# Optimization experiments

Hardware: AMD Instinct MI355X
Metric: run time of the kernel (lower is better)

Reference implementation:

```python
import jax, jax.numpy as jnp
import numpy as np

EMB = 384
H = 6
D = 64
B = 256
T = 256


def setup_inputs() -> dict:
    key = jax.random.key(0)
    ks = jax.random.split(key, 6)
    s = 1.0 / np.sqrt(EMB)
    return {
        "x": jax.random.normal(ks[0], (B, T, EMB), dtype=jnp.float32),
        "wq": jax.random.normal(ks[1], (H, EMB, D), dtype=jnp.float32) * s,
        "wk": jax.random.normal(ks[2], (H, EMB, D), dtype=jnp.float32) * s,
        "wv": jax.random.normal(ks[3], (H, EMB, D), dtype=jnp.float32) * s,
        "w_proj": jax.random.normal(ks[4], (H * D, EMB), dtype=jnp.float32) * s,
        "b_proj": jax.random.normal(ks[5], (EMB,), dtype=jnp.float32) * 0.01,
    }


def reference(x, wq, wk, wv, w_proj, b_proj):
    # x: [B, T, E]; per-head projections stacked over H (dropout in eval mode)
    q = jnp.einsum("bte,hed->bhtd", x, wq)
    k = jnp.einsum("bte,hed->bhtd", x, wk)
    v = jnp.einsum("bte,hed->bhtd", x, wv)
    scale = q.shape[-1] ** -0.5
    scores = jnp.einsum("bhqd,bhkd->bhqk", q, k) * scale  # [B,H,T,T]
    tq = q.shape[2]
    causal = jnp.tril(jnp.ones((tq, tq), dtype=bool))
    scores = jnp.where(causal, scores, -jnp.inf)
    att = jax.nn.softmax(scores, axis=-1)
    out = jnp.einsum("bhqk,bhkd->bhqd", att, v)  # [B,H,T,D]
    out = out.transpose(0, 2, 1, 3).reshape(x.shape[0], tq, -1)  # concat heads
    return out @ w_proj + b_proj
```

## Files before the change

### kernel.cpp

```cpp
#include <hip/hip_runtime.h>
#include <hip/hip_bf16.h>


#define Bn 256
#define Tn 256
#define En 384
#define Hn 6
#define Dn 64

typedef __bf16 bf16x8 __attribute__((ext_vector_type(8)));
typedef float f32x4 __attribute__((ext_vector_type(4)));
typedef unsigned short u16x8 __attribute__((ext_vector_type(8)));

static __device__ __forceinline__ unsigned short f2bf(float f) {
    unsigned int u = __builtin_bit_cast(unsigned int, f);
    u += 0x7fffu + ((u >> 16) & 1u);
    return (unsigned short)(u >> 16);
}

static __device__ __forceinline__ f32x4 mfma16(bf16x8 a, bf16x8 b, f32x4 c) {
    return __builtin_amdgcn_mfma_f32_16x16x32_bf16(a, b, c, 0, 0, 0);
}

static __device__ __forceinline__ void glds16(const unsigned short* g, unsigned short* l) {
    __builtin_amdgcn_global_load_lds(
        (const __attribute__((address_space(1))) unsigned int*)g,
        (__attribute__((address_space(3))) unsigned int*)l, 16, 0, 0);
}

__global__ __launch_bounds__(256) void prep_kernel(
    const float* __restrict__ wq, const float* __restrict__ wk,
    const float* __restrict__ wv, const float* __restrict__ wp,
    unsigned short* __restrict__ wt, unsigned short* __restrict__ wpt) {
    const int NW = 3 * Hn * Dn * En;
    const int NP = En * En;
    int idx = blockIdx.x * 256 + threadIdx.x;
    if (idx < NW) {
        int e = idx % En;
        int d = (idx / En) % Dn;
        int h = (idx / (En * Dn)) % Hn;
        int t = idx / (En * Dn * Hn);
        const float* src = (t == 0) ? wq : (t == 1) ? wk : wv;
        wt[idx] = f2bf(src[(h * En + e) * Dn + d]);
    } else if (idx < NW + NP) {
        int j = idx - NW;
        int k = j % En;
        int n = j / En;
        wpt[j] = f2bf(wp[k * En + n]);
    }
}

__global__ __launch_bounds__(256) void xcast_kernel(
    const float* __restrict__ x, unsigned short* __restrict__ xb) {
    size_t i = ((size_t)blockIdx.x * 256 + threadIdx.x) * 8;
    float4 f0 = *(const float4*)(x + i);
    float4 f1 = *(const float4*)(x + i + 4);
    u16x8 p;
    p[0] = f2bf(f0.x); p[1] = f2bf(f0.y); p[2] = f2bf(f0.z); p[3] = f2bf(f0.w);
    p[4] = f2bf(f1.x); p[5] = f2bf(f1.y); p[6] = f2bf(f1.z); p[7] = f2bf(f1.w);
    *(u16x8*)(xb + i) = p;
}

__global__ __launch_bounds__(256) void qkv_gemm(
    const unsigned short* __restrict__ xb, const unsigned short* __restrict__ wt,
    unsigned short* __restrict__ Qo, unsigned short* __restrict__ Ko,
    unsigned short* __restrict__ Vt) {
    __shared__ unsigned short As[2][128][64];
    __shared__ unsigned short Bs[2][192][64];

    const int h = blockIdx.x;
    const int m0 = blockIdx.y * 128;

    const int tid = threadIdx.x;
    const int wave = tid >> 6, lane = tid & 63;
    const int quad = lane >> 4, l16 = lane & 15;
    const int mw = (wave >> 1) * 64, nw = (wave & 1) * 96;

    f32x4 acc[4][6];
#pragma unroll
    for (int i = 0; i < 4; ++i)
#pragma unroll
        for (int j = 0; j < 6; ++j) acc[i][j] = (f32x4){0.f, 0.f, 0.f, 0.f};

    const int lr = lane >> 3;
    const int js = (lane & 7) ^ lr;

    const unsigned short* ga[4];
#pragma unroll
    for (int i = 0; i < 4; ++i)
        ga[i] = xb + (size_t)(m0 + wave * 32 + i * 8 + lr) * En + js * 8;
    const unsigned short* gb[6];
#pragma unroll
    for (int i = 0; i < 6; ++i) {
        int n = wave * 48 + i * 8 + lr;
        gb[i] = wt + (size_t)(((n >> 6) * Hn + h) * Dn + (n & 63)) * En + js * 8;
    }

#define QKV_STAGE(buf, koff)                                              \
    do {                                                                  \
        _Pragma("unroll") for (int i = 0; i < 4; ++i)                     \
            glds16(ga[i] + (koff), &As[buf][wave * 32 + i * 8][0]);       \
        _Pragma("unroll") for (int i = 0; i < 6; ++i)                     \
            glds16(gb[i] + (koff), &Bs[buf][wave * 48 + i * 8][0]);       \
    } while (0)

    QKV_STAGE(0, 0);
    __syncthreads();

    int cur = 0;
    for (int kb = 0; kb < 6; ++kb) {
        if (kb < 5) QKV_STAGE(cur ^ 1, (kb + 1) * 64);

#pragma unroll
        for (int ks = 0; ks < 2; ++ks) {
            bf16x8 a[4], b[6];
            const int ps = ((ks * 4 + quad) ^ (l16 & 7)) * 8;
#pragma unroll
            for (int mi = 0; mi < 4; ++mi)
                a[mi] = *(const bf16x8*)&As[cur][mw + mi * 16 + l16][ps];
#pragma unroll
            for (int ni = 0; ni < 6; ++ni)
                b[ni] = *(const bf16x8*)&Bs[cur][nw + ni * 16 + l16][ps];
#pragma unroll
            for (int mi = 0; mi < 4; ++mi)
#pragma unroll
                for (int ni = 0; ni < 6; ++ni) acc[mi][ni] = mfma16(a[mi], b[ni], acc[mi][ni]);
        }
        if (kb < 5) {
            __syncthreads();
            cur ^= 1;
        }
    }
#undef QKV_STAGE

    const int b = m0 >> 8, tbase = m0 & 255;
    unsigned short* qkbase[2] = {
        Qo + (size_t)((b * Hn + h) * Tn) * Dn,
        Ko + (size_t)((b * Hn + h) * Tn) * Dn };
    unsigned short* vdst = Vt + (size_t)((b * Hn + h) * Dn) * Tn;
#pragma unroll
    for (int ni = 0; ni < 6; ++ni) {
        const int ng = nw + ni * 16;
        const int tensor = ng >> 6;
        const int d = (ng & 63) + l16;
        if (tensor < 2) {
            unsigned short* dst = qkbase[tensor];
#pragma unroll
            for (int mi = 0; mi < 4; ++mi)
#pragma unroll
                for (int r = 0; r < 4; ++r) {
                    int t = tbase + mw + mi * 16 + quad * 4 + r;
                    dst[t * Dn + d] = f2bf(acc[mi][ni][r]);
                }
        } else {
#pragma unroll
            for (int mi = 0; mi < 4; ++mi) {
                int t0 = tbase + mw + mi * 16 + quad * 4;
                ushort4 pk;
                pk.x = f2bf(acc[mi][ni][0]);
                pk.y = f2bf(acc[mi][ni][1]);
                pk.z = f2bf(acc[mi][ni][2]);
                pk.w = f2bf(acc[mi][ni][3]);
                *(ushort4*)&vdst[d * Tn + t0] = pk;
            }
        }
    }
}

__global__ __launch_bounds__(256) void attn_kernel(
    const unsigned short* __restrict__ Q, const unsigned short* __restrict__ K,
    const unsigned short* __restrict__ Vt, unsigned short* __restrict__ attout) {
    __shared__ unsigned short Kt[256][64];
    __shared__ unsigned short Vl[64][256];
    __shared__ unsigned short P[4][16][72];

    const int h = blockIdx.x, b = blockIdx.y;
    const unsigned short* Qb = Q + (size_t)((b * Hn + h) * Tn) * Dn;
    const unsigned short* Kb = K + (size_t)((b * Hn + h) * Tn) * Dn;
    const unsigned short* Vb = Vt + (size_t)((b * Hn + h) * Dn) * Tn;

    const int tid = threadIdx.x;
    const int wave = tid >> 6, lane = tid & 63;
    const int quad = lane >> 4, l16 = lane & 15;

    {
        const unsigned short* kg = Kb + (size_t)(lane >> 3) * Dn + ((lane & 7) ^ (lane >> 3)) * 8;
#pragma unroll
        for (int i = 0; i < 8; ++i) {
            const int c = wave * 8 + i;
            glds16(kg + (size_t)c * 8 * Dn, &Kt[c * 8][0]);
        }
#pragma unroll
        for (int i = 0; i < 8; ++i) {
            const int c = wave * 8 + i;
            const int d = c * 2 + (lane >> 5);
            const int j = (lane & 31) ^ (d & 7);
            glds16(Vb + (size_t)d * Tn + j * 8, &Vl[c * 2][0]);
        }
    }
    __syncthreads();

    const float cexp = 0.125f * 1.44269504f;
    const int grp[4] = {wave, 7 - wave, 8 + wave, 15 - wave};

    for (int gi = 0; gi < 4; ++gi) {
        const int g = grp[gi];
        const int q0 = g * 16;

        bf16x8 aq[2];
#pragma unroll
        for (int ks = 0; ks < 2; ++ks)
            aq[ks] = *(const bf16x8*)&Qb[(q0 + l16) * Dn + ks * 32 + quad * 8];

        f32x4 O[4];
#pragma unroll
        for (int i = 0; i < 4; ++i) O[i] = (f32x4){0.f, 0.f, 0.f, 0.f};
        float rsum[4] = {0.f, 0.f, 0.f, 0.f};

        const int ktmax = g >> 2;
        for (int kt = 0; kt <= ktmax; ++kt) {
            f32x4 S[4];
#pragma unroll
            for (int i = 0; i < 4; ++i) S[i] = (f32x4){0.f, 0.f, 0.f, 0.f};
#pragma unroll
            for (int ks = 0; ks < 2; ++ks)
#pragma unroll
                for (int ni = 0; ni < 4; ++ni) {
                    bf16x8 bk = *(const bf16x8*)
                        &Kt[kt * 64 + ni * 16 + l16][(((ks * 4 + quad) ^ (l16 & 7)) * 8)];
                    S[ni] = mfma16(aq[ks], bk, S[ni]);
                }

#pragma unroll
            for (int ni = 0; ni < 4; ++ni)
#pragma unroll
                for (int r = 0; r < 4; ++r) {
                    int col = kt * 64 + ni * 16 + l16;
                    float p = exp2f(S[ni][r] * cexp);
                    p = (col > q0 + quad * 4 + r) ? 0.f : p;
                    rsum[r] += p;
                    P[wave][quad * 4 + r][ni * 16 + l16] = f2bf(p);
                }

#pragma unroll
            for (int ks = 0; ks < 2; ++ks) {
                bf16x8 ap = *(const bf16x8*)&P[wave][l16][ks * 32 + quad * 8];
#pragma unroll
                for (int ni = 0; ni < 4; ++ni) {
                    bf16x8 bv = *(const bf16x8*)
                        &Vl[ni * 16 + l16][(((kt * 8 + ks * 4 + quad) ^ (l16 & 7)) * 8)];
                    O[ni] = mfma16(ap, bv, O[ni]);
                }
            }
        }

#pragma unroll
        for (int r = 0; r < 4; ++r) {
            float s = rsum[r];
            s += __shfl_xor(s, 1);
            s += __shfl_xor(s, 2);
            s += __shfl_xor(s, 4);
            s += __shfl_xor(s, 8);
            rsum[r] = s;
        }

#pragma unroll
        for (int r = 0; r < 4; ++r) {
            float inv = 1.0f / rsum[r];
#pragma unroll
            for (int ni = 0; ni < 4; ++ni)
                P[wave][quad * 4 + r][ni * 16 + l16] = f2bf(O[ni][r] * inv);
        }
        const int row = lane >> 2;
        const int colc = (lane & 3) * 16;
        unsigned short* dst = attout + (size_t)(b * Tn + q0 + row) * (Hn * Dn) + h * Dn + colc;
        *(uint4*)dst = *(const uint4*)&P[wave][row][colc];
        *(uint4*)(dst + 8) = *(const uint4*)&P[wave][row][colc + 8];
    }
}

__global__ __launch_bounds__(256) void proj_gemm(
    const unsigned short* __restrict__ attout, const unsigned short* __restrict__ wpt,
    const float* __restrict__ bproj, float* __restrict__ out) {
    __shared__ unsigned short As[2][128][64];
    __shared__ unsigned short Bs[2][128][64];

    const int n0 = blockIdx.x * 128;
    const int m0 = blockIdx.y * 128;

    const int tid = threadIdx.x;
    const int wave = tid >> 6, lane = tid & 63;
    const int quad = lane >> 4, l16 = lane & 15;
    const int mw = (wave >> 1) * 64, nw = (wave & 1) * 64;

    f32x4 acc[4][4];
#pragma unroll
    for (int i = 0; i < 4; ++i)
#pragma unroll
        for (int j = 0; j < 4; ++j) acc[i][j] = (f32x4){0.f, 0.f, 0.f, 0.f};

    const int lr = lane >> 3;
    const int js = (lane & 7) ^ lr;

    const unsigned short* ga[4];
    const unsigned short* gb[4];
#pragma unroll
    for (int i = 0; i < 4; ++i) {
        ga[i] = attout + (size_t)(m0 + wave * 32 + i * 8 + lr) * En + js * 8;
        gb[i] = wpt + (size_t)(n0 + wave * 32 + i * 8 + lr) * En + js * 8;
    }

#define PROJ_STAGE(buf, koff)                                             \
    do {                                                                  \
        _Pragma("unroll") for (int i = 0; i < 4; ++i)                     \
            glds16(ga[i] + (koff), &As[buf][wave * 32 + i * 8][0]);       \
        _Pragma("unroll") for (int i = 0; i < 4; ++i)                     \
            glds16(gb[i] + (koff), &Bs[buf][wave * 32 + i * 8][0]);       \
    } while (0)

    PROJ_STAGE(0, 0);
    __syncthreads();

    int cur = 0;
    for (int kb = 0; kb < 6; ++kb) {
        if (kb < 5) PROJ_STAGE(cur ^ 1, (kb + 1) * 64);

#pragma unroll
        for (int ks = 0; ks < 2; ++ks) {
            bf16x8 a[4], bb[4];
            const int ps = ((ks * 4 + quad) ^ (l16 & 7)) * 8;
#pragma unroll
            for (int mi = 0; mi < 4; ++mi)
                a[mi] = *(const bf16x8*)&As[cur][mw + mi * 16 + l16][ps];
#pragma unroll
            for (int ni = 0; ni < 4; ++ni)
                bb[ni] = *(const bf16x8*)&Bs[cur][nw + ni * 16 + l16][ps];
#pragma unroll
            for (int mi = 0; mi < 4; ++mi)
#pragma unroll
                for (int ni = 0; ni < 4; ++ni) acc[mi][ni] = mfma16(a[mi], bb[ni], acc[mi][ni]);
        }
        if (kb < 5) {
            __syncthreads();
            cur ^= 1;
        }
    }
#undef PROJ_STAGE

#pragma unroll
    for (int mi = 0; mi < 4; ++mi)
#pragma unroll
        for (int ni = 0; ni < 4; ++ni)
#pragma unroll
            for (int r = 0; r < 4; ++r) {
                int row = m0 + mw + mi * 16 + quad * 4 + r;
                int col = n0 + nw + ni * 16 + l16;
                out[(size_t)row * En + col] = acc[mi][ni][r] + bproj[col];
            }
}

extern "C" void kernel_launch(void* const* d_in, const int* in_sizes, int n_in,
                              void* d_out, int out_size, void* d_ws, size_t ws_size,
                              hipStream_t stream) {
    const float* x  = (const float*)d_in[0];
    const float* wq = (const float*)d_in[1];
    const float* wk = (const float*)d_in[2];
    const float* wv = (const float*)d_in[3];
    const float* wp = (const float*)d_in[4];
    const float* bp = (const float*)d_in[5];
    float* out = (float*)d_out;

    char* ws = (char*)d_ws;
    const size_t WT_OFF  = 0;
    const size_t WPT_OFF = WT_OFF + 884736;
    const size_t Q_OFF   = WPT_OFF + 294912;
    const size_t K_OFF   = Q_OFF + 50331648ull;
    const size_t VT_OFF  = K_OFF + 50331648ull;
    const size_t XB_OFF  = VT_OFF + 50331648ull;

    unsigned short* wt   = (unsigned short*)(ws + WT_OFF);
    unsigned short* wpt  = (unsigned short*)(ws + WPT_OFF);
    unsigned short* Qd   = (unsigned short*)(ws + Q_OFF);
    unsigned short* Kd   = (unsigned short*)(ws + K_OFF);
    unsigned short* Vtd  = (unsigned short*)(ws + VT_OFF);
    unsigned short* xbd  = (unsigned short*)(ws + XB_OFF);
    unsigned short* ao   = xbd;

    prep_kernel<<<2304, 256, 0, stream>>>(wq, wk, wv, wp, wt, wpt);
    xcast_kernel<<<12288, 256, 0, stream>>>(x, xbd);
    qkv_gemm<<<dim3(Hn, 512), 256, 0, stream>>>(xbd, wt, Qd, Kd, Vtd);
    attn_kernel<<<dim3(Hn, Bn), 256, 0, stream>>>(Qd, Kd, Vtd, ao);
    proj_gemm<<<dim3(3, 512), 256, 0, stream>>>(ao, wpt, bp, out);
}
```

Before: 379.4 us.

## Triple-buffer QKV and projection GEMMs with vmcnt waits and XCD-aware block swizzle

Both GEMM kernels move from double to triple-buffered LDS staging. Each iteration waits with explicit s_waitcnt vmcnt counts and a raw s_barrier instead of __syncthreads, so two tiles of loads stay in flight. Launches become 1D with a block-index swizzle that spreads blocks across the 8 XCDs, aiming for better L2 locality. The larger LDS footprint (72KB and 48KB) may lower occupancy, and the hand-tuned vmcnt values depend on how many loads glds16 issues.

Result: no change. 380.7 us (+0.3%).

```diff
diff --git a/kernel.cpp b/kernel.cpp
--- a/kernel.cpp
+++ b/kernel.cpp
@@ -65,11 +65,13 @@
     const unsigned short* __restrict__ xb, const unsigned short* __restrict__ wt,
     unsigned short* __restrict__ Qo, unsigned short* __restrict__ Ko,
     unsigned short* __restrict__ Vt) {
-    __shared__ unsigned short As[2][128][64];
-    __shared__ unsigned short Bs[2][192][64];
-
-    const int h = blockIdx.x;
-    const int m0 = blockIdx.y * 128;
+    __shared__ unsigned short As[3][128][64];
+    __shared__ unsigned short Bs[3][192][64];
+
+    const int bid = blockIdx.x;
+    const int swz = (bid & 7) * 384 + (bid >> 3);
+    const int h = swz % Hn;
+    const int m0 = (swz / Hn) * 128;
 
     const int tid = threadIdx.x;
     const int wave = tid >> 6, lane = tid & 63;
@@ -105,12 +107,16 @@
     } while (0)
 
     QKV_STAGE(0, 0);
-    __syncthreads();
-
-    int cur = 0;
+    QKV_STAGE(1, 64);
+
+#pragma unroll
     for (int kb = 0; kb < 6; ++kb) {
-        if (kb < 5) QKV_STAGE(cur ^ 1, (kb + 1) * 64);
-
+        if (kb < 5) asm volatile("s_waitcnt vmcnt(10)" ::: "memory");
+        else        asm volatile("s_waitcnt vmcnt(0)" ::: "memory");
+        __builtin_amdgcn_s_barrier();
+        if (kb < 4) QKV_STAGE((kb + 2) % 3, (kb + 2) * 64);
+
+        const int cur = kb % 3;
 #pragma unroll
         for (int ks = 0; ks < 2; ++ks) {
             bf16x8 a[4], b[6];
@@ -125,10 +131,6 @@
             for (int mi = 0; mi < 4; ++mi)
 #pragma unroll
                 for (int ni = 0; ni < 6; ++ni) acc[mi][ni] = mfma16(a[mi], b[ni], acc[mi][ni]);
-        }
-        if (kb < 5) {
-            __syncthreads();
-            cur ^= 1;
         }
     }
 #undef QKV_STAGE
@@ -282,11 +284,13 @@
 __global__ __launch_bounds__(256) void proj_gemm(
     const unsigned short* __restrict__ attout, const unsigned short* __restrict__ wpt,
     const float* __restrict__ bproj, float* __restrict__ out) {
-    __shared__ unsigned short As[2][128][64];
-    __shared__ unsigned short Bs[2][128][64];
-
-    const int n0 = blockIdx.x * 128;
-    const int m0 = blockIdx.y * 128;
+    __shared__ unsigned short As[3][128][64];
+    __shared__ unsigned short Bs[3][128][64];
+
+    const int bid = blockIdx.x;
+    const int swz = (bid & 7) * 192 + (bid >> 3);
+    const int n0 = (swz % 3) * 128;
+    const int m0 = (swz / 3) * 128;
 
     const int tid = threadIdx.x;
     const int wave = tid >> 6, lane = tid & 63;
@@ -319,12 +323,16 @@
     } while (0)
 
     PROJ_STAGE(0, 0);
-    __syncthreads();
-
-    int cur = 0;
+    PROJ_STAGE(1, 64);
+
+#pragma unroll
     for (int kb = 0; kb < 6; ++kb) {
-        if (kb < 5) PROJ_STAGE(cur ^ 1, (kb + 1) * 64);
-
+        if (kb < 5) asm volatile("s_waitcnt vmcnt(8)" ::: "memory");
+        else        asm volatile("s_waitcnt vmcnt(0)" ::: "memory");
+        __builtin_amdgcn_s_barrier();
+        if (kb < 4) PROJ_STAGE((kb + 2) % 3, (kb + 2) * 64);
+
+        const int cur = kb % 3;
 #pragma unroll
         for (int ks = 0; ks < 2; ++ks) {
             bf16x8 a[4], bb[4];
@@ -339,10 +347,6 @@
             for (int mi = 0; mi < 4; ++mi)
 #pragma unroll
                 for (int ni = 0; ni < 4; ++ni) acc[mi][ni] = mfma16(a[mi], bb[ni], acc[mi][ni]);
-        }
-        if (kb < 5) {
-            __syncthreads();
-            cur ^= 1;
         }
     }
 #undef PROJ_STAGE
@@ -388,7 +392,7 @@
 
     prep_kernel<<<2304, 256, 0, stream>>>(wq, wk, wv, wp, wt, wpt);
     xcast_kernel<<<12288, 256, 0, stream>>>(x, xbd);
-    qkv_gemm<<<dim3(Hn, 512), 256, 0, stream>>>(xbd, wt, Qd, Kd, Vtd);
+    qkv_gemm<<<3072, 256, 0, stream>>>(xbd, wt, Qd, Kd, Vtd);
     attn_kernel<<<dim3(Hn, Bn), 256, 0, stream>>>(Qd, Kd, Vtd, ao);
-    proj_gemm<<<dim3(3, 512), 256, 0, stream>>>(ao, wpt, bp, out);
-}
+    proj_gemm<<<1536, 256, 0, stream>>>(ao, wpt, bp, out);
+}
```
